# Optimization experiments

Measured on AMD Instinct MI355X. Metric: run time of the kernel, lower is better.

The kernel has to match this reference:

```python
import jax, jax.numpy as jnp
import numpy as np

B, S, D, H = 8, 1024, 1024, 16
DH = D // H
LN_EPS = 1e-5


def setup_inputs() -> dict:
    key = jax.random.key(0)
    ks = jax.random.split(key, 8)
    scale = 1.0 / np.sqrt(D)
    return {
        "x": jax.random.normal(ks[0], (B, S, D), dtype=jnp.float32),
        "lengths": jax.random.randint(ks[1], (B,), 0, 1024),
        "Wq": jax.random.normal(ks[2], (D, D), dtype=jnp.float32) * scale,
        "bq": jax.random.normal(ks[3], (D,), dtype=jnp.float32) * 0.01,
        "Wk": jax.random.normal(ks[4], (D, D), dtype=jnp.float32) * scale,
        "bk": jax.random.normal(ks[5], (D,), dtype=jnp.float32) * 0.01,
        "Wv": jax.random.normal(ks[6], (D, D), dtype=jnp.float32) * scale,
        "bv": jax.random.normal(ks[7], (D,), dtype=jnp.float32) * 0.01,
        "gamma": jnp.ones((D,), dtype=jnp.float32),
        "beta": jnp.zeros((D,), dtype=jnp.float32),
    }


def _split_heads(t):
    # [B,S,D] -> permute(0,2,1) -> [B,D,S] -> view(B*H,DH,S) -> permute(0,2,1)
    # equivalent to contiguous channel-chunk head split:
    return t.reshape(B, S, H, DH).transpose(0, 2, 1, 3).reshape(B * H, S, DH)


def reference(x, lengths, Wq, bq, Wk, bk, Wv, bv, gamma, beta):
    q = _split_heads(x @ Wq.T + bq)  # [B*H, S, DH]
    k = _split_heads(x @ Wk.T + bk)
    v = _split_heads(x @ Wv.T + bv)

    # Faithful bug reproduction: lengths has B entries but Q/K/V have B*H
    # rows, so only rows 0..B-1 of the flattened (B*H) dim get zeroed.
    pos = jnp.arange(S)
    row_mask = jnp.ones((B * H, S), dtype=bool)
    row_mask = row_mask.at[:B].set(pos[None, :] < lengths[:, None])
    m = row_mask[:, :, None].astype(q.dtype)
    q, k, v = q * m, k * m, v * m

    scores = jnp.einsum("bsd,btd->bst", q, k)  # [B*H, S, S]
    scores = jnp.where(scores == 0, jnp.asarray(1e-10, scores.dtype), scores)
    scores = scores / jnp.sqrt(jnp.asarray(D, scores.dtype))  # d_k = d_model
    attn = jax.nn.softmax(scores, axis=2)
    ctx = jnp.einsum("bst,btd->bsd", attn, v)  # [B*H, S, DH]

    # merge heads: inverse of _split_heads
    ctx = ctx.reshape(B, H, S, DH).transpose(0, 2, 1, 3).reshape(B, S, D)

    out = ctx + x  # dropout p=0.0
    mu = jnp.mean(out, axis=-1, keepdims=True)
    var = jnp.var(out, axis=-1, keepdims=True)
    out = (out - mu) * jax.lax.rsqrt(var + LN_EPS) * gamma + beta
    return out
```

## Files before the change

kernel.cpp:

```cpp
#include <hip/hip_runtime.h>

#define B_ 8
#define S_ 1024
#define D_ 1024
#define H_ 16
#define DH_ 64

typedef __attribute__((ext_vector_type(4))) float f32x4;
typedef __attribute__((ext_vector_type(8))) short short8;

__device__ __forceinline__ unsigned short f32_to_bf16_rne(float f) {
    union { float f; unsigned int u; } c; c.f = f;
    unsigned int u = c.u;
    unsigned int r = u + 0x7FFFu + ((u >> 16) & 1u);
    return (unsigned short)(r >> 16);
}

__device__ __forceinline__ void gl_lds16(const unsigned short* g, const unsigned short* l) {
    __builtin_amdgcn_global_load_lds((const __attribute__((address_space(1))) unsigned int*)g,
                                     (__attribute__((address_space(3))) unsigned int*)l, 16, 0, 0);
}

__global__ __launch_bounds__(256) void cvt_all(const float* __restrict__ x,
                                               const float* __restrict__ Wq,
                                               const float* __restrict__ Wk,
                                               const float* __restrict__ Wv,
                                               unsigned short* __restrict__ xb,
                                               unsigned short* __restrict__ wb) {
    int bid = blockIdx.x;
    const float* src; unsigned short* dst; long i;
    if (bid < 4096) {
        src = x; dst = xb; i = (long)bid * 256 + threadIdx.x;
    } else {
        int wbid = bid - 4096;
        int z = wbid >> 9;
        src = (z == 0) ? Wq : ((z == 1) ? Wk : Wv);
        dst = wb + (size_t)z * D_ * D_;
        i = (long)(wbid & 511) * 256 + threadIdx.x;
    }
    const float4* s4 = reinterpret_cast<const float4*>(src) + i * 2;
    float4 a = s4[0], b = s4[1];
    short8 o;
    o[0] = (short)f32_to_bf16_rne(a.x); o[1] = (short)f32_to_bf16_rne(a.y);
    o[2] = (short)f32_to_bf16_rne(a.z); o[3] = (short)f32_to_bf16_rne(a.w);
    o[4] = (short)f32_to_bf16_rne(b.x); o[5] = (short)f32_to_bf16_rne(b.y);
    o[6] = (short)f32_to_bf16_rne(b.z); o[7] = (short)f32_to_bf16_rne(b.w);
    reinterpret_cast<short8*>(dst)[i] = o;
}

__global__ __launch_bounds__(512, 2) void gemm_qkv(const unsigned short* __restrict__ X,
                                                   const unsigned short* __restrict__ Wall,
                                                   const float* __restrict__ bq,
                                                   const float* __restrict__ bk,
                                                   const float* __restrict__ bv,
                                                   const int* __restrict__ lengths,
                                                   unsigned short* __restrict__ QKV,
                                                   unsigned short* __restrict__ Vt) {
    extern __shared__ unsigned short smem[];
    const int STG = 20480;

    const int bid = blockIdx.x;
    const int xcd = bid & 7, loc = bid >> 3;
    const int mt = xcd * 4 + (loc & 3);
    const int nt = loc >> 2;
    const int m0 = mt * 256, n0 = nt * 128;
    const int tid = threadIdx.x;
    const int lane = tid & 63;
    const int w = tid >> 6;
    const int wm = (w >> 1) * 64, wn = (w & 1) * 64;
    const int g = lane >> 4;

    int aoff[4];
    #pragma unroll
    for (int i = 0; i < 4; i++) {
        int arow = wm + i * 16 + (lane & 15);
        aoff[i] = arow * 32 + ((g ^ ((arow >> 1) & 3)) * 8);
    }
    const int dB = (wn - wm) * 32;

    const unsigned short* xsrc[2];
    const unsigned short* wsrc[3];
    #pragma unroll
    for (int p = 0; p < 2; p++) {
        int row = p * 128 + w * 16 + (lane >> 2);
        int c = (lane & 3) ^ ((row >> 1) & 3);
        xsrc[p] = &X[(size_t)(m0 + row) * D_ + c * 8];
    }
    {
        int row = w * 16 + (lane >> 2);
        int c = (lane & 3) ^ ((row >> 1) & 3);
        const unsigned short* wb0 = &Wall[(size_t)(n0 + row) * D_ + c * 8];
        wsrc[0] = wb0;
        wsrc[1] = wb0 + (size_t)D_ * D_;
        wsrc[2] = wb0 + (size_t)2 * D_ * D_;
    }

    auto stage = [&](int s) {
        unsigned short* ab = smem + s * STG;
        #pragma unroll
        for (int p = 0; p < 2; p++) {
            gl_lds16(xsrc[p], ab + (p * 512 + w * 64) * 8);
            xsrc[p] += 32;
        }
        unsigned short* bb = ab + 8192;
        #pragma unroll
        for (int p = 0; p < 3; p++) {
            gl_lds16(wsrc[p], bb + (p * 512 + w * 64) * 8);
            wsrc[p] += 32;
        }
    };

    f32x4 acc[3][4][4] = {};

    stage(0);
    stage(1);
    int cur = 0;
    for (int t = 0; t < 32; t++) {
        if (t < 31) asm volatile("s_waitcnt vmcnt(5)" ::: "memory");
        else        asm volatile("s_waitcnt vmcnt(0)" ::: "memory");
        __builtin_amdgcn_s_barrier();
        if (t < 30) stage(cur ? cur - 1 : 2);
        const unsigned short* Ab = smem + cur * STG;
        const unsigned short* Bb = Ab + 8192 + dB;
        short8 af[4];
        #pragma unroll
        for (int i = 0; i < 4; i++)
            af[i] = *reinterpret_cast<const short8*>(&Ab[aoff[i]]);
        #pragma unroll
        for (int z = 0; z < 3; z++) {
            short8 bf[4];
            #pragma unroll
            for (int j = 0; j < 4; j++)
                bf[j] = *reinterpret_cast<const short8*>(&Bb[z * 4096 + aoff[j]]);
            #pragma unroll
            for (int i = 0; i < 4; i++)
                #pragma unroll
                for (int j = 0; j < 4; j++)
                    acc[z][i][j] = __builtin_amdgcn_mfma_f32_16x16x32_bf16(af[i], bf[j], acc[z][i][j], 0, 0, 0);
        }
        cur = (cur == 2) ? 0 : cur + 1;
    }

    #pragma unroll
    for (int z = 0; z < 2; z++) {
        unsigned short* Out = QKV + (size_t)z * (B_ * S_) * D_;
        const float* bias = z ? bk : bq;
        #pragma unroll
        for (int j = 0; j < 4; j++) {
            int ncol = n0 + wn + j * 16 + (lane & 15);
            float bval = bias[ncol];
            int len = (ncol < 512) ? lengths[ncol >> 6] : (1 << 30);
            #pragma unroll
            for (int i = 0; i < 4; i++) {
                int mbase = m0 + wm + i * 16 + ((lane >> 4) << 2);
                #pragma unroll
                for (int r = 0; r < 4; r++) {
                    int m = mbase + r;
                    float v = acc[z][i][j][r] + bval;
                    if (m < S_ && ncol < 512 && m >= len) v = 0.f;
                    Out[(size_t)m * D_ + ncol] = f32_to_bf16_rne(v);
                }
            }
        }
    }
    {
        #pragma unroll
        for (int j = 0; j < 4; j++) {
            int ncol = n0 + wn + j * 16 + (lane & 15);
            float bval = bv[ncol];
            int len = (ncol < 512) ? lengths[ncol >> 6] : (1 << 30);
            int h = ncol >> 6, dh = ncol & 63;
            #pragma unroll
            for (int i = 0; i < 4; i++) {
                int mbase = m0 + wm + i * 16 + ((lane >> 4) << 2);
                int b = mbase >> 10, s = mbase & 1023;
                unsigned short v4[4];
                #pragma unroll
                for (int r = 0; r < 4; r++) {
                    int m = mbase + r;
                    float v = acc[2][i][j][r] + bval;
                    if (m < S_ && ncol < 512 && m >= len) v = 0.f;
                    v4[r] = f32_to_bf16_rne(v);
                }
                *reinterpret_cast<uint2*>(&Vt[((size_t)((b * 16 + h) * 64 + dh)) * S_ + s]) =
                    *reinterpret_cast<uint2*>(v4);
            }
        }
    }
}

__global__ __launch_bounds__(256, 4) void attn_kernel(const unsigned short* __restrict__ QKV,
                                                      const unsigned short* __restrict__ Vt,
                                                      unsigned short* __restrict__ Ctxb) {
    const int id = blockIdx.x;
    const int xcd = id & 7, seq = id >> 3;
    const int qt = seq & 7;
    const int bh = ((seq >> 3) << 3) | xcd;
    const int b = bh >> 4, h = bh & 15;
    const int tid = threadIdx.x, lane = tid & 63, w = tid >> 6;
    const int qcol = lane & 15, g = lane >> 4;

    __shared__ unsigned short Ks[2][64 * 64];
    __shared__ unsigned short Vs[2][64 * 64];

    const unsigned short* Qg = QKV + (size_t)(b * S_) * D_ + h * DH_;
    const unsigned short* Kg = Qg + (size_t)(B_ * S_) * D_;
    const unsigned short* Vg = Vt + (size_t)bh * DH_ * S_;

    const int q0w = qt * 128 + w * 16;

    short8 qfA[2], qfB[2];
    {
        const unsigned short* qa = Qg + (size_t)(q0w + qcol) * D_ + g * 8;
        qfA[0] = *reinterpret_cast<const short8*>(qa);
        qfA[1] = *reinterpret_cast<const short8*>(qa + 32);
        const unsigned short* qb = Qg + (size_t)(q0w + 64 + qcol) * D_ + g * 8;
        qfB[0] = *reinterpret_cast<const short8*>(qb);
        qfB[1] = *reinterpret_cast<const short8*>(qb + 32);
    }

    float lA = 0.f, lB = 0.f;
    f32x4 caccA[4] = {}, caccB[4] = {};

    const unsigned short* kp0; const unsigned short* kp1;
    const unsigned short* vp0; const unsigned short* vp1;
    {
        int i0 = (w * 2 + 0) * 64 + lane;
        int r0 = i0 >> 3, c0 = (i0 & 7) ^ (r0 & 7);
        kp0 = Kg + (size_t)r0 * D_ + c0 * 8;
        vp0 = Vg + (size_t)r0 * S_ + c0 * 8;
        int i1 = (w * 2 + 1) * 64 + lane;
        int r1 = i1 >> 3, c1 = (i1 & 7) ^ (r1 & 7);
        kp1 = Kg + (size_t)r1 * D_ + c1 * 8;
        vp1 = Vg + (size_t)r1 * S_ + c1 * 8;
    }
    unsigned short* kd0[2] = { &Ks[0][(w * 2 + 0) * 512], &Ks[1][(w * 2 + 0) * 512] };
    unsigned short* kd1[2] = { &Ks[0][(w * 2 + 1) * 512], &Ks[1][(w * 2 + 1) * 512] };
    unsigned short* vd0[2] = { &Vs[0][(w * 2 + 0) * 512], &Vs[1][(w * 2 + 0) * 512] };
    unsigned short* vd1[2] = { &Vs[0][(w * 2 + 1) * 512], &Vs[1][(w * 2 + 1) * 512] };

    auto stage = [&](int bf) {
        gl_lds16(kp0, kd0[bf]); gl_lds16(kp1, kd1[bf]);
        gl_lds16(vp0, vd0[bf]); gl_lds16(vp1, vd1[bf]);
        kp0 += 64 * D_; kp1 += 64 * D_;
        vp0 += 64;      vp1 += 64;
    };

    const float C2 = 0.04508422004083421f;
    const float MB = 11.54156171223618f;

    union F8 { unsigned int u[4]; short8 s; };

    stage(0);
    #pragma unroll 2
    for (int t = 0; t < 16; t++) {
        __syncthreads();
        if (t < 15) stage((t + 1) & 1);
        const unsigned short* Kb = Ks[t & 1];
        const unsigned short* Vb = Vs[t & 1];

        f32x4 sA[4] = {}, sB[4] = {};
        __builtin_amdgcn_s_setprio(1);
        #pragma unroll
        for (int ks = 0; ks < 2; ks++) {
            #pragma unroll
            for (int ni = 0; ni < 4; ni++) {
                int krow = ni * 16 + qcol;
                int slot = (ks * 4 + g) ^ (krow & 7);
                short8 kf = *reinterpret_cast<const short8*>(&Kb[krow * 64 + slot * 8]);
                sA[ni] = __builtin_amdgcn_mfma_f32_16x16x32_bf16(kf, qfA[ks], sA[ni], 0, 0, 0);
                sB[ni] = __builtin_amdgcn_mfma_f32_16x16x32_bf16(kf, qfB[ks], sB[ni], 0, 0, 0);
            }
        }
        __builtin_amdgcn_s_setprio(0);

        F8 pkA0, pkA1, pkB0, pkB1;
        {
            float p[16];
            #pragma unroll
            for (int ni = 0; ni < 4; ni++)
                #pragma unroll
                for (int r = 0; r < 4; r++)
                    p[ni * 4 + r] = __builtin_amdgcn_exp2f(__builtin_fmaf(sA[ni][r], C2, -MB));
            lA += ((p[0] + p[1]) + (p[2] + p[3])) + ((p[4] + p[5]) + (p[6] + p[7]))
                + ((p[8] + p[9]) + (p[10] + p[11])) + ((p[12] + p[13]) + (p[14] + p[15]));
            unsigned int Wa[4], Wb[4];
            #pragma unroll
            for (int ni = 0; ni < 4; ni++) {
                asm("v_cvt_pk_bf16_f32 %0, %1, %2" : "=v"(Wa[ni]) : "v"(p[ni * 4 + 0]), "v"(p[ni * 4 + 1]));
                asm("v_cvt_pk_bf16_f32 %0, %1, %2" : "=v"(Wb[ni]) : "v"(p[ni * 4 + 2]), "v"(p[ni * 4 + 3]));
            }
            unsigned int a0 = Wa[0], a1 = Wa[1], b0 = Wb[0], b1 = Wb[1];
            unsigned int c0 = Wa[2], c1 = Wa[3], d0 = Wb[2], d1 = Wb[3];
            asm("v_permlane32_swap_b32 %0, %1" : "+v"(a0), "+v"(a1));
            asm("v_permlane16_swap_b32 %0, %1" : "+v"(a0), "+v"(a1));
            asm("v_permlane32_swap_b32 %0, %1" : "+v"(b0), "+v"(b1));
            asm("v_permlane16_swap_b32 %0, %1" : "+v"(b0), "+v"(b1));
            asm("v_permlane32_swap_b32 %0, %1" : "+v"(c0), "+v"(c1));
            asm("v_permlane16_swap_b32 %0, %1" : "+v"(c0), "+v"(c1));
            asm("v_permlane32_swap_b32 %0, %1" : "+v"(d0), "+v"(d1));
            asm("v_permlane16_swap_b32 %0, %1" : "+v"(d0), "+v"(d1));
            pkA0.u[0] = a0; pkA0.u[1] = b0; pkA0.u[2] = a1; pkA0.u[3] = b1;
            pkA1.u[0] = c0; pkA1.u[1] = d0; pkA1.u[2] = c1; pkA1.u[3] = d1;
        }
        {
            float p[16];
            #pragma unroll
            for (int ni = 0; ni < 4; ni++)
                #pragma unroll
                for (int r = 0; r < 4; r++)
                    p[ni * 4 + r] = __builtin_amdgcn_exp2f(__builtin_fmaf(sB[ni][r], C2, -MB));
            lB += ((p[0] + p[1]) + (p[2] + p[3])) + ((p[4] + p[5]) + (p[6] + p[7]))
                + ((p[8] + p[9]) + (p[10] + p[11])) + ((p[12] + p[13]) + (p[14] + p[15]));
            unsigned int Wa[4], Wb[4];
            #pragma unroll
            for (int ni = 0; ni < 4; ni++) {
                asm("v_cvt_pk_bf16_f32 %0, %1, %2" : "=v"(Wa[ni]) : "v"(p[ni * 4 + 0]), "v"(p[ni * 4 + 1]));
                asm("v_cvt_pk_bf16_f32 %0, %1, %2" : "=v"(Wb[ni]) : "v"(p[ni * 4 + 2]), "v"(p[ni * 4 + 3]));
            }
            unsigned int a0 = Wa[0], a1 = Wa[1], b0 = Wb[0], b1 = Wb[1];
            unsigned int c0 = Wa[2], c1 = Wa[3], d0 = Wb[2], d1 = Wb[3];
            asm("v_permlane32_swap_b32 %0, %1" : "+v"(a0), "+v"(a1));
            asm("v_permlane16_swap_b32 %0, %1" : "+v"(a0), "+v"(a1));
            asm("v_permlane32_swap_b32 %0, %1" : "+v"(b0), "+v"(b1));
            asm("v_permlane16_swap_b32 %0, %1" : "+v"(b0), "+v"(b1));
            asm("v_permlane32_swap_b32 %0, %1" : "+v"(c0), "+v"(c1));
            asm("v_permlane16_swap_b32 %0, %1" : "+v"(c0), "+v"(c1));
            asm("v_permlane32_swap_b32 %0, %1" : "+v"(d0), "+v"(d1));
            asm("v_permlane16_swap_b32 %0, %1" : "+v"(d0), "+v"(d1));
            pkB0.u[0] = a0; pkB0.u[1] = b0; pkB0.u[2] = a1; pkB0.u[3] = b1;
            pkB1.u[0] = c0; pkB1.u[1] = d0; pkB1.u[2] = c1; pkB1.u[3] = d1;
        }

        __builtin_amdgcn_s_setprio(1);
        #pragma unroll
        for (int ks = 0; ks < 2; ks++) {
            short8 pfA = ks ? pkA1.s : pkA0.s;
            short8 pfB = ks ? pkB1.s : pkB0.s;
            #pragma unroll
            for (int ni = 0; ni < 4; ni++) {
                int vrow = ni * 16 + qcol;
                int slot = (ks * 4 + g) ^ (vrow & 7);
                short8 vf = *reinterpret_cast<const short8*>(&Vb[vrow * 64 + slot * 8]);
                caccA[ni] = __builtin_amdgcn_mfma_f32_16x16x32_bf16(pfA, vf, caccA[ni], 0, 0, 0);
                caccB[ni] = __builtin_amdgcn_mfma_f32_16x16x32_bf16(pfB, vf, caccB[ni], 0, 0, 0);
            }
        }
        __builtin_amdgcn_s_setprio(0);
    }

    lA += __shfl_xor(lA, 16, 64);
    lA += __shfl_xor(lA, 32, 64);
    lB += __shfl_xor(lB, 16, 64);
    lB += __shfl_xor(lB, 32, 64);

    #pragma unroll
    for (int r = 0; r < 4; r++) {
        float la = __shfl(lA, (g << 2) + r, 64);
        float lb = __shfl(lB, (g << 2) + r, 64);
        float invA = 1.f / la, invB = 1.f / lb;
        int qrowA = q0w + (g << 2) + r;
        int qrowB = qrowA + 64;
        #pragma unroll
        for (int ni = 0; ni < 4; ni++) {
            int dh = ni * 16 + qcol;
            Ctxb[(size_t)(b * S_ + qrowA) * D_ + h * DH_ + dh] = f32_to_bf16_rne(caccA[ni][r] * invA);
            Ctxb[(size_t)(b * S_ + qrowB) * D_ + h * DH_ + dh] = f32_to_bf16_rne(caccB[ni][r] * invB);
        }
    }
}

__global__ __launch_bounds__(256) void ln_kernel(const unsigned short* __restrict__ Ctxb,
                                                 const unsigned short* __restrict__ Xb,
                                                 const float* __restrict__ gamma,
                                                 const float* __restrict__ beta,
                                                 float* __restrict__ out) {
    const int row = blockIdx.x;
    const int tid = threadIdx.x;
    const int lane = tid & 63, w = tid >> 6;

    ushort4 c4 = reinterpret_cast<const ushort4*>(Ctxb + (size_t)row * D_)[tid];
    ushort4 x4 = reinterpret_cast<const ushort4*>(Xb + (size_t)row * D_)[tid];
    float4 v;
    v.x = __uint_as_float((unsigned)c4.x << 16) + __uint_as_float((unsigned)x4.x << 16);
    v.y = __uint_as_float((unsigned)c4.y << 16) + __uint_as_float((unsigned)x4.y << 16);
    v.z = __uint_as_float((unsigned)c4.z << 16) + __uint_as_float((unsigned)x4.z << 16);
    v.w = __uint_as_float((unsigned)c4.w << 16) + __uint_as_float((unsigned)x4.w << 16);

    float s = v.x + v.y + v.z + v.w;
    float ss = v.x * v.x + v.y * v.y + v.z * v.z + v.w * v.w;
    for (int off = 1; off < 64; off <<= 1) {
        s += __shfl_xor(s, off, 64);
        ss += __shfl_xor(ss, off, 64);
    }
    __shared__ float sbuf[4], ssbuf[4];
    if (lane == 0) { sbuf[w] = s; ssbuf[w] = ss; }
    __syncthreads();
    s = sbuf[0] + sbuf[1] + sbuf[2] + sbuf[3];
    ss = ssbuf[0] + ssbuf[1] + ssbuf[2] + ssbuf[3];

    float mean = s * (1.f / D_);
    float var = ss * (1.f / D_) - mean * mean;
    float rstd = rsqrtf(var + 1e-5f);

    const float4 gm = reinterpret_cast<const float4*>(gamma)[tid];
    const float4 bt = reinterpret_cast<const float4*>(beta)[tid];
    float4 o;
    o.x = (v.x - mean) * rstd * gm.x + bt.x;
    o.y = (v.y - mean) * rstd * gm.y + bt.y;
    o.z = (v.z - mean) * rstd * gm.z + bt.z;
    o.w = (v.w - mean) * rstd * gm.w + bt.w;
    reinterpret_cast<float4*>(out + (size_t)row * D_)[tid] = o;
}

extern "C" void kernel_launch(void* const* d_in, const int* in_sizes, int n_in,
                              void* d_out, int out_size, void* d_ws, size_t ws_size,
                              hipStream_t stream) {
    const float* x       = (const float*)d_in[0];
    const int*   lengths = (const int*)d_in[1];
    const float* Wq      = (const float*)d_in[2];
    const float* bq      = (const float*)d_in[3];
    const float* Wk      = (const float*)d_in[4];
    const float* bk      = (const float*)d_in[5];
    const float* Wv      = (const float*)d_in[6];
    const float* bv      = (const float*)d_in[7];
    const float* gamma   = (const float*)d_in[8];
    const float* beta    = (const float*)d_in[9];
    float* out = (float*)d_out;

    char* ws = (char*)d_ws;
    unsigned short* xb    = (unsigned short*)(ws);
    unsigned short* Wball = (unsigned short*)(ws + 16777216);
    unsigned short* QKV   = (unsigned short*)(ws + 23068672);
    unsigned short* Vt    = (unsigned short*)(ws + 56623104);
    unsigned short* Ctxb  = (unsigned short*)(ws + 73400320);

    (void)hipFuncSetAttribute((const void*)gemm_qkv,
                              hipFuncAttributeMaxDynamicSharedMemorySize, 122880);

    cvt_all<<<5632, 256, 0, stream>>>(x, Wq, Wk, Wv, xb, Wball);

    gemm_qkv<<<256, 512, 122880, stream>>>(xb, Wball, bq, bk, bv, lengths, QKV, Vt);

    attn_kernel<<<1024, 256, 0, stream>>>(QKV, Vt, Ctxb);

    ln_kernel<<<8192, 256, 0, stream>>>(Ctxb, xb, gamma, beta, out);
}
```

Measured before the change: 137.7 us.

## Split QKV GEMM into Q/K pass and separate V pass with ping-pong scheduling

The fused QKV GEMM previously held three accumulator sets and staged X plus three weight tiles per K step. It now runs Q and K together with two accumulator sets, writes them out, then runs a second pipelined loop for V with a wider K step of 64 and an 8-way XOR swizzle. Both loops split each K step into two halves, each with its own barriers, s_setprio around the MFMA bursts and interleaved global-to-LDS staging. Launch bounds drop to one block per CU and LDS grows to 144 KB. The intent is to cut register pressure and overlap loads with MFMA, at the cost of re-reading X for the V pass and lower occupancy.

```diff
diff --git a/kernel.cpp b/kernel.cpp
--- a/kernel.cpp
+++ b/kernel.cpp
@@ -48,7 +48,7 @@
     reinterpret_cast<short8*>(dst)[i] = o;
 }
 
-__global__ __launch_bounds__(512, 2) void gemm_qkv(const unsigned short* __restrict__ X,
+__global__ __launch_bounds__(512, 1) void gemm_qkv(const unsigned short* __restrict__ X,
                                                    const unsigned short* __restrict__ Wall,
                                                    const float* __restrict__ bq,
                                                    const float* __restrict__ bk,
@@ -57,7 +57,8 @@
                                                    unsigned short* __restrict__ QKV,
                                                    unsigned short* __restrict__ Vt) {
     extern __shared__ unsigned short smem[];
-    const int STG = 20480;
+    const int STG1 = 16384;
+    const int STG2 = 24576;
 
     const int bid = blockIdx.x;
     const int xcd = bid & 7, loc = bid >> 3;
@@ -70,75 +71,88 @@
     const int wm = (w >> 1) * 64, wn = (w & 1) * 64;
     const int g = lane >> 4;
 
-    int aoff[4];
+    int aoffQ[4], boffQ[4];
     #pragma unroll
     for (int i = 0; i < 4; i++) {
-        int arow = wm + i * 16 + (lane & 15);
-        aoff[i] = arow * 32 + ((g ^ ((arow >> 1) & 3)) * 8);
-    }
-    const int dB = (wn - wm) * 32;
-
-    const unsigned short* xsrc[2];
-    const unsigned short* wsrc[3];
+        int ar = wm + i * 16 + (lane & 15);
+        aoffQ[i] = ar * 32 + ((g ^ ((ar >> 1) & 3)) * 8);
+        int br = wn + i * 16 + (lane & 15);
+        boffQ[i] = 8192 + br * 32 + ((g ^ ((br >> 1) & 3)) * 8);
+    }
+
+    const unsigned short* xs[2];
+    const unsigned short* ws[2];
     #pragma unroll
     for (int p = 0; p < 2; p++) {
-        int row = p * 128 + w * 16 + (lane >> 2);
+        int row = p * 128 + (tid >> 2);
         int c = (lane & 3) ^ ((row >> 1) & 3);
-        xsrc[p] = &X[(size_t)(m0 + row) * D_ + c * 8];
+        xs[p] = &X[(size_t)(m0 + row) * D_ + c * 8];
     }
     {
-        int row = w * 16 + (lane >> 2);
+        int row = tid >> 2;
         int c = (lane & 3) ^ ((row >> 1) & 3);
-        const unsigned short* wb0 = &Wall[(size_t)(n0 + row) * D_ + c * 8];
-        wsrc[0] = wb0;
-        wsrc[1] = wb0 + (size_t)D_ * D_;
-        wsrc[2] = wb0 + (size_t)2 * D_ * D_;
-    }
-
-    auto stage = [&](int s) {
-        unsigned short* ab = smem + s * STG;
+        ws[0] = &Wall[(size_t)(n0 + row) * D_ + c * 8];
+        ws[1] = ws[0] + (size_t)D_ * D_;
+    }
+
+    auto stageA = [&](int s) {
+        unsigned short* ab = smem + s * STG1;
         #pragma unroll
         for (int p = 0; p < 2; p++) {
-            gl_lds16(xsrc[p], ab + (p * 512 + w * 64) * 8);
-            xsrc[p] += 32;
-        }
-        unsigned short* bb = ab + 8192;
-        #pragma unroll
-        for (int p = 0; p < 3; p++) {
-            gl_lds16(wsrc[p], bb + (p * 512 + w * 64) * 8);
-            wsrc[p] += 32;
+            gl_lds16(xs[p], ab + (p * 512 + w * 64) * 8);
+            xs[p] += 32;
         }
     };
-
-    f32x4 acc[3][4][4] = {};
-
-    stage(0);
-    stage(1);
-    int cur = 0;
+    auto stageB = [&](int s) {
+        unsigned short* bb = smem + s * STG1 + 8192;
+        #pragma unroll
+        for (int z2 = 0; z2 < 2; z2++) {
+            gl_lds16(ws[z2], bb + z2 * 4096 + w * 512);
+            ws[z2] += 32;
+        }
+    };
+
+    f32x4 acc[2][4][4] = {};
+
+    stageA(0); stageB(0);
+    stageA(1); stageB(1);
+    asm volatile("s_waitcnt vmcnt(4)" ::: "memory");
+    __builtin_amdgcn_s_barrier();
+
     for (int t = 0; t < 32; t++) {
-        if (t < 31) asm volatile("s_waitcnt vmcnt(5)" ::: "memory");
+        const unsigned short* Ab = smem + (t % 3) * STG1;
+        short8 af[4], bfq[4];
+        #pragma unroll
+        for (int i = 0; i < 4; i++) af[i]  = *reinterpret_cast<const short8*>(&Ab[aoffQ[i]]);
+        #pragma unroll
+        for (int j = 0; j < 4; j++) bfq[j] = *reinterpret_cast<const short8*>(&Ab[boffQ[j]]);
+        if (t < 30) stageA((t + 2) % 3);
+        __builtin_amdgcn_s_barrier();
+        asm volatile("s_waitcnt lgkmcnt(0)" ::: "memory");
+        __builtin_amdgcn_s_setprio(1);
+        #pragma unroll
+        for (int i = 0; i < 4; i++)
+            #pragma unroll
+            for (int j = 0; j < 4; j++)
+                acc[0][i][j] = __builtin_amdgcn_mfma_f32_16x16x32_bf16(af[i], bfq[j], acc[0][i][j], 0, 0, 0);
+        __builtin_amdgcn_s_setprio(0);
+        __builtin_amdgcn_s_barrier();
+        short8 bfk[4];
+        #pragma unroll
+        for (int j = 0; j < 4; j++) bfk[j] = *reinterpret_cast<const short8*>(&Ab[boffQ[j] + 4096]);
+        if (t < 30) stageB((t + 2) % 3);
+        if (t < 30) asm volatile("s_waitcnt vmcnt(4)" ::: "memory");
         else        asm volatile("s_waitcnt vmcnt(0)" ::: "memory");
         __builtin_amdgcn_s_barrier();
-        if (t < 30) stage(cur ? cur - 1 : 2);
-        const unsigned short* Ab = smem + cur * STG;
-        const unsigned short* Bb = Ab + 8192 + dB;
-        short8 af[4];
+        asm volatile("s_waitcnt lgkmcnt(0)" ::: "memory");
+        __builtin_amdgcn_s_setprio(1);
         #pragma unroll
         for (int i = 0; i < 4; i++)
-            af[i] = *reinterpret_cast<const short8*>(&Ab[aoff[i]]);
-        #pragma unroll
-        for (int z = 0; z < 3; z++) {
-            short8 bf[4];
             #pragma unroll
             for (int j = 0; j < 4; j++)
-                bf[j] = *reinterpret_cast<const short8*>(&Bb[z * 4096 + aoff[j]]);
-            #pragma unroll
-            for (int i = 0; i < 4; i++)
-                #pragma unroll
-                for (int j = 0; j < 4; j++)
-                    acc[z][i][j] = __builtin_amdgcn_mfma_f32_16x16x32_bf16(af[i], bf[j], acc[z][i][j], 0, 0, 0);
-        }
-        cur = (cur == 2) ? 0 : cur + 1;
+                acc[1][i][j] = __builtin_amdgcn_mfma_f32_16x16x32_bf16(af[i], bfk[j], acc[1][i][j], 0, 0, 0);
+        __builtin_amdgcn_s_setprio(0);
+        __builtin_amdgcn_s_barrier();
     }
 
     #pragma unroll
@@ -163,6 +177,97 @@
             }
         }
     }
+
+    const unsigned short* Wv = Wall + (size_t)2 * D_ * D_;
+
+    int aoffV[2][4], boffV[2][4];
+    #pragma unroll
+    for (int ks = 0; ks < 2; ks++)
+        #pragma unroll
+        for (int i = 0; i < 4; i++) {
+            int ar = wm + i * 16 + (lane & 15);
+            aoffV[ks][i] = ar * 64 + (((ks * 4 + g) ^ (ar & 7)) * 8);
+            int br = wn + i * 16 + (lane & 15);
+            boffV[ks][i] = 16384 + br * 64 + (((ks * 4 + g) ^ (br & 7)) * 8);
+        }
+
+    const unsigned short* xv[4];
+    const unsigned short* wv[2];
+    #pragma unroll
+    for (int p = 0; p < 4; p++) {
+        int row = p * 64 + w * 8 + (lane >> 3);
+        int c = (lane & 7) ^ (row & 7);
+        xv[p] = &X[(size_t)(m0 + row) * D_ + c * 8];
+    }
+    #pragma unroll
+    for (int p = 0; p < 2; p++) {
+        int row = p * 64 + w * 8 + (lane >> 3);
+        int c = (lane & 7) ^ (row & 7);
+        wv[p] = &Wv[(size_t)(n0 + row) * D_ + c * 8];
+    }
+
+    auto stageVA = [&](int s) {
+        unsigned short* ab = smem + s * STG2;
+        #pragma unroll
+        for (int p = 0; p < 4; p++) {
+            gl_lds16(xv[p], ab + (p * 512 + w * 64) * 8);
+            xv[p] += 64;
+        }
+    };
+    auto stageVB = [&](int s) {
+        unsigned short* bb = smem + s * STG2 + 16384;
+        #pragma unroll
+        for (int p = 0; p < 2; p++) {
+            gl_lds16(wv[p], bb + (p * 512 + w * 64) * 8);
+            wv[p] += 64;
+        }
+    };
+
+    f32x4 accv[4][4] = {};
+
+    stageVA(0); stageVB(0);
+    stageVA(1); stageVB(1);
+    asm volatile("s_waitcnt vmcnt(6)" ::: "memory");
+    __builtin_amdgcn_s_barrier();
+
+    for (int t = 0; t < 16; t++) {
+        const unsigned short* Av = smem + (t % 3) * STG2;
+        short8 af0[4], bf0[4];
+        #pragma unroll
+        for (int i = 0; i < 4; i++) af0[i] = *reinterpret_cast<const short8*>(&Av[aoffV[0][i]]);
+        #pragma unroll
+        for (int j = 0; j < 4; j++) bf0[j] = *reinterpret_cast<const short8*>(&Av[boffV[0][j]]);
+        if (t < 14) stageVA((t + 2) % 3);
+        __builtin_amdgcn_s_barrier();
+        asm volatile("s_waitcnt lgkmcnt(0)" ::: "memory");
+        __builtin_amdgcn_s_setprio(1);
+        #pragma unroll
+        for (int i = 0; i < 4; i++)
+            #pragma unroll
+            for (int j = 0; j < 4; j++)
+                accv[i][j] = __builtin_amdgcn_mfma_f32_16x16x32_bf16(af0[i], bf0[j], accv[i][j], 0, 0, 0);
+        __builtin_amdgcn_s_setprio(0);
+        __builtin_amdgcn_s_barrier();
+        short8 af1[4], bf1[4];
+        #pragma unroll
+        for (int i = 0; i < 4; i++) af1[i] = *reinterpret_cast<const short8*>(&Av[aoffV[1][i]]);
+        #pragma unroll
+        for (int j = 0; j < 4; j++) bf1[j] = *reinterpret_cast<const short8*>(&Av[boffV[1][j]]);
+        if (t < 14) stageVB((t + 2) % 3);
+        if (t < 14) asm volatile("s_waitcnt vmcnt(6)" ::: "memory");
+        else        asm volatile("s_waitcnt vmcnt(0)" ::: "memory");
+        __builtin_amdgcn_s_barrier();
+        asm volatile("s_waitcnt lgkmcnt(0)" ::: "memory");
+        __builtin_amdgcn_s_setprio(1);
+        #pragma unroll
+        for (int i = 0; i < 4; i++)
+            #pragma unroll
+            for (int j = 0; j < 4; j++)
+                accv[i][j] = __builtin_amdgcn_mfma_f32_16x16x32_bf16(af1[i], bf1[j], accv[i][j], 0, 0, 0);
+        __builtin_amdgcn_s_setprio(0);
+        __builtin_amdgcn_s_barrier();
+    }
+
     {
         #pragma unroll
         for (int j = 0; j < 4; j++) {
@@ -178,7 +283,7 @@
                 #pragma unroll
                 for (int r = 0; r < 4; r++) {
                     int m = mbase + r;
-                    float v = acc[2][i][j][r] + bval;
+                    float v = accv[i][j][r] + bval;
                     if (m < S_ && ncol < 512 && m >= len) v = 0.f;
                     v4[r] = f32_to_bf16_rne(v);
                 }
@@ -436,11 +541,11 @@
     unsigned short* Ctxb  = (unsigned short*)(ws + 73400320);
 
     (void)hipFuncSetAttribute((const void*)gemm_qkv,
-                              hipFuncAttributeMaxDynamicSharedMemorySize, 122880);
+                              hipFuncAttributeMaxDynamicSharedMemorySize, 147456);
 
     cvt_all<<<5632, 256, 0, stream>>>(x, Wq, Wk, Wv, xb, Wball);
 
-    gemm_qkv<<<256, 512, 122880, stream>>>(xb, Wball, bq, bk, bv, lengths, QKV, Vt);
+    gemm_qkv<<<256, 512, 147456, stream>>>(xb, Wball, bq, bk, bv, lengths, QKV, Vt);
 
     attn_kernel<<<1024, 256, 0, stream>>>(QKV, Vt, Ctxb);
 
```

Result: faster. 131.1 us (-4.8%).
